# Performance work log

Measured on AMD Instinct MI355X. Metric: run time of the kernel, lower is better.

Reference implementation:

```python
import jax, jax.numpy as jnp
import numpy as np

EPS = 1e-5

def gelu(x):
    return jax.nn.gelu(x, approximate=False)  # torch nn.GELU default = exact erf

def bn(x, g, b, m, v):
    # eval-mode BatchNorm1d with running stats; broadcasts over batch axis
    return (x - m) * jax.lax.rsqrt(v + EPS) * g + b

def ln(x, g, b):
    mu = jnp.mean(x, axis=-1, keepdims=True)
    var = jnp.var(x, axis=-1, keepdims=True)
    return (x - mu) * jax.lax.rsqrt(var + EPS) * g + b

def setup_inputs() -> dict:
    B, D, H, E, C = 4096, 512, 1024, 16, 20  # combined dim D = wifi(256)+rfid(256)
    key = jax.random.key(0)
    ks = iter(jax.random.split(key, 40))
    n = lambda shape, s=0.02: jax.random.normal(next(ks), shape, dtype=jnp.float32) * s
    u = lambda shape: jax.random.uniform(next(ks), shape, dtype=jnp.float32, minval=0.5, maxval=1.5)
    inp = {
        'wifi_feat': jax.random.normal(next(ks), (B, 256), dtype=jnp.float32),
        'rfid_feat': jax.random.normal(next(ks), (B, 256), dtype=jnp.float32),
        # gate: Linear(512,1024) -> LayerNorm -> GELU -> Linear(1024,16) -> Softmax
        'gate_w1': n((D, 1024)), 'gate_b1': n((1024,)),
        'gate_ln_g': 1.0 + n((1024,)), 'gate_ln_b': n((1024,)),
        'gate_w2': n((1024, E)), 'gate_b2': n((E,)),
        # experts stacked on leading E axis
        'exp_w1': n((E, D, H)), 'exp_b1': n((E, H)),
        'exp_bn1_g': 1.0 + n((E, H)), 'exp_bn1_b': n((E, H)), 'exp_bn1_m': n((E, H), 0.1), 'exp_bn1_v': u((E, H)),
        'exp_w2': n((E, H, H)), 'exp_b2': n((E, H)),
        'exp_bn2_g': 1.0 + n((E, H)), 'exp_bn2_b': n((E, H)), 'exp_bn2_m': n((E, H), 0.1), 'exp_bn2_v': u((E, H)),
        # final head: Linear(1024,512) -> BN -> GELU -> Linear(512,20)
        'fin_w1': n((H, 512)), 'fin_b1': n((512,)),
        'fin_bn_g': 1.0 + n((512,)), 'fin_bn_b': n((512,)), 'fin_bn_m': n((512,), 0.1), 'fin_bn_v': u((512,)),
        'fin_w2': n((512, C)), 'fin_b2': n((C,)),
    }
    return inp

def reference(wifi_feat, rfid_feat,
              gate_w1, gate_b1, gate_ln_g, gate_ln_b, gate_w2, gate_b2,
              exp_w1, exp_b1, exp_bn1_g, exp_bn1_b, exp_bn1_m, exp_bn1_v,
              exp_w2, exp_b2, exp_bn2_g, exp_bn2_b, exp_bn2_m, exp_bn2_v,
              fin_w1, fin_b1, fin_bn_g, fin_bn_b, fin_bn_m, fin_bn_v,
              fin_w2, fin_b2):
    TOPK = 4
    combined = jnp.concatenate([wifi_feat, rfid_feat], axis=1)  # [B, 512]
    # gate
    g = gelu(ln(combined @ gate_w1 + gate_b1, gate_ln_g, gate_ln_b))
    gate = jax.nn.softmax(g @ gate_w2 + gate_b2, axis=1)  # [B, E]
    topk_gate, topk_idx = jax.lax.top_k(gate, TOPK)  # sorted, matches torch.topk
    topk_gate = jax.nn.softmax(topk_gate, axis=1)  # [B, K]
    # dense all-expert stack (faithful to original torch.stack over experts)
    h = jnp.einsum('bi,eih->ebh', combined, exp_w1) + exp_b1[:, None, :]  # [E,B,H]
    h = gelu(bn(h, exp_bn1_g[:, None, :], exp_bn1_b[:, None, :], exp_bn1_m[:, None, :], exp_bn1_v[:, None, :]))
    h = jnp.einsum('ebh,eho->ebo', h, exp_w2) + exp_b2[:, None, :]
    h = gelu(bn(h, exp_bn2_g[:, None, :], exp_bn2_b[:, None, :], exp_bn2_m[:, None, :], exp_bn2_v[:, None, :]))
    expert_outputs = jnp.transpose(h, (1, 0, 2))  # [B, E, H]
    selected = jnp.take_along_axis(expert_outputs, topk_idx[:, :, None], axis=1)  # [B,K,H]
    fused = jnp.einsum('bkd,bk->bd', selected, topk_gate)  # [B, H]
    # final head
    o = gelu(bn(fused @ fin_w1 + fin_b1, fin_bn_g, fin_bn_b, fin_bn_m, fin_bn_v))
    return o @ fin_w2 + fin_b2  # [B, num_classes]
```

## Files before the change

### kernel.cpp

```cpp
#include <hip/hip_runtime.h>


#define EPSN 1e-5f

typedef __attribute__((ext_vector_type(8))) short v8s;
typedef __attribute__((ext_vector_type(4))) float v4f;

typedef const unsigned int __attribute__((address_space(1)))* gas_u32;
typedef unsigned int __attribute__((address_space(3)))* las_u32;

__device__ __forceinline__ void glds16(const void* g, const void* l) {
    __builtin_amdgcn_global_load_lds((gas_u32)(uintptr_t)g, (las_u32)(uintptr_t)l, 16, 0, 0);
}

__device__ __forceinline__ float gelu_f(float x) {
    return 0.5f * x * (1.0f + erff(x * 0.70710678118654752440f));
}
__device__ __forceinline__ unsigned short f2bf(float x) {
    unsigned int u = __float_as_uint(x);
    u += 0x7fffu + ((u >> 16) & 1u);
    return (unsigned short)(u >> 16);
}
__device__ __forceinline__ float bf2f(unsigned short u) {
    return __uint_as_float(((unsigned int)u) << 16);
}

__global__ __launch_bounds__(256) void concat_kernel(const float4* __restrict__ wifi,
                                                     const float4* __restrict__ rfid,
                                                     float4* __restrict__ comb,
                                                     ushort4* __restrict__ cbf) {
    int gid = blockIdx.x * 256 + threadIdx.x;
    int b = gid >> 7, c = gid & 127;
    float4 v = (c < 64) ? wifi[b * 64 + c] : rfid[b * 64 + (c - 64)];
    comb[gid] = v;
    ushort4 o;
    o.x = f2bf(v.x); o.y = f2bf(v.y); o.z = f2bf(v.z); o.w = f2bf(v.w);
    cbf[gid] = o;
}

__global__ __launch_bounds__(256) void transpose_f2b(const float* __restrict__ in,
                                                     unsigned short* __restrict__ out,
                                                     int K, int N) {
    __shared__ float t[64][65];
    int e = blockIdx.z;
    int n0 = blockIdx.x << 6, k0 = blockIdx.y << 6;
    const float* ie = in + (long)e * K * N;
    unsigned short* oe = out + (long)e * N * K;
    int tid = threadIdx.x;
    int rr = tid >> 4, cc = (tid & 15) << 2;
#pragma unroll
    for (int p = 0; p < 4; ++p) {
        int k = (p << 4) + rr;
        float4 v = *(const float4*)(ie + (long)(k0 + k) * N + n0 + cc);
        t[k][cc + 0] = v.x; t[k][cc + 1] = v.y; t[k][cc + 2] = v.z; t[k][cc + 3] = v.w;
    }
    __syncthreads();
    int n = tid >> 2, kq = (tid & 3) << 4;
    unsigned short u[16];
#pragma unroll
    for (int j = 0; j < 16; ++j) u[j] = f2bf(t[kq + j][n]);
    uint4* dst = (uint4*)(oe + (long)(n0 + n) * K + k0 + kq);
    dst[0] = ((const uint4*)u)[0];
    dst[1] = ((const uint4*)u)[1];
}

__global__ __launch_bounds__(256) void gate_gemm(
    const float* __restrict__ A, int lda,
    const float* __restrict__ W,
    const float* __restrict__ bias,
    float* __restrict__ out, int ldo, int N, int K)
{
    const int m0 = blockIdx.y << 7;
    const int n0 = blockIdx.x << 6;
    __shared__ float As[16][132];
    __shared__ float Bs[16][68];
    const int tid = threadIdx.x;
    const int ty = tid >> 4, tx = tid & 15;

    const int arow = tid >> 1;
    const int akq  = (tid & 1) << 3;
    const float* Aptr = A + (long)(m0 + arow) * lda + akq;
    const int bkr = tid >> 4;
    const int bnq = (tid & 15) << 2;
    const float* Bptr = W + (long)bkr * N + n0 + bnq;

    float acc[8][4] = {};
    for (int k0 = 0; k0 < K; k0 += 16) {
        float4 a0 = *(const float4*)(Aptr + k0);
        float4 a1 = *(const float4*)(Aptr + k0 + 4);
        float4 bv = *(const float4*)(Bptr + (long)k0 * N);
        As[akq + 0][arow] = a0.x; As[akq + 1][arow] = a0.y;
        As[akq + 2][arow] = a0.z; As[akq + 3][arow] = a0.w;
        As[akq + 4][arow] = a1.x; As[akq + 5][arow] = a1.y;
        As[akq + 6][arow] = a1.z; As[akq + 7][arow] = a1.w;
        *(float4*)&Bs[bkr][bnq] = bv;
        __syncthreads();
#pragma unroll
        for (int kk = 0; kk < 16; ++kk) {
            float4 af0 = *(const float4*)&As[kk][ty << 3];
            float4 af1 = *(const float4*)&As[kk][(ty << 3) + 4];
            float4 bf = *(const float4*)&Bs[kk][tx << 2];
            const float a8[8] = {af0.x, af0.y, af0.z, af0.w, af1.x, af1.y, af1.z, af1.w};
            const float b4[4] = {bf.x, bf.y, bf.z, bf.w};
#pragma unroll
            for (int i = 0; i < 8; ++i)
#pragma unroll
                for (int j = 0; j < 4; ++j)
                    acc[i][j] = fmaf(a8[i], b4[j], acc[i][j]);
        }
        __syncthreads();
    }
#pragma unroll
    for (int i = 0; i < 8; ++i) {
        int r = m0 + (ty << 3) + i;
        int c0 = n0 + (tx << 2);
        float4 v;
        v.x = acc[i][0] + bias[c0 + 0];
        v.y = acc[i][1] + bias[c0 + 1];
        v.z = acc[i][2] + bias[c0 + 2];
        v.w = acc[i][3] + bias[c0 + 3];
        *(float4*)(out + (long)r * ldo + c0) = v;
    }
}

__global__ __launch_bounds__(256) void ln_topk_kernel(
    const float* __restrict__ g,
    const float* __restrict__ lng, const float* __restrict__ lnb,
    const float* __restrict__ w2, const float* __restrict__ b2,
    float* __restrict__ wout, int* __restrict__ rows_, int* __restrict__ counts)
{
    __shared__ float gs[1024];
    __shared__ float red[16][17];
    __shared__ float rs[4], rq[4];
    const int b = blockIdx.x;
    const int tid = threadIdx.x;
    const int c = tid << 2;

    float4 v = *(const float4*)(g + (long)b * 1024 + c);
    float s = v.x + v.y + v.z + v.w;
    float q = v.x * v.x + v.y * v.y + v.z * v.z + v.w * v.w;
    for (int off = 32; off > 0; off >>= 1) {
        s += __shfl_down(s, off);
        q += __shfl_down(q, off);
    }
    int wid = tid >> 6;
    if ((tid & 63) == 0) { rs[wid] = s; rq[wid] = q; }
    __syncthreads();
    float S = rs[0] + rs[1] + rs[2] + rs[3];
    float Q = rq[0] + rq[1] + rq[2] + rq[3];
    float mu = S * (1.0f / 1024.0f);
    float var = Q * (1.0f / 1024.0f) - mu * mu;
    float rstd = rsqrtf(var + EPSN);
    gs[c + 0] = gelu_f((v.x - mu) * rstd * lng[c + 0] + lnb[c + 0]);
    gs[c + 1] = gelu_f((v.y - mu) * rstd * lng[c + 1] + lnb[c + 1]);
    gs[c + 2] = gelu_f((v.z - mu) * rstd * lng[c + 2] + lnb[c + 2]);
    gs[c + 3] = gelu_f((v.w - mu) * rstd * lng[c + 3] + lnb[c + 3]);
    __syncthreads();

    const int e = tid & 15, chunk = tid >> 4;
    float p = 0.f;
#pragma unroll 8
    for (int i = 0; i < 64; ++i) {
        int idx = (chunk << 6) + i;
        p = fmaf(gs[idx], w2[(idx << 4) + e], p);
    }
    red[chunk][e] = p;
    __syncthreads();

    if (tid < 64) {
        float logit = -1e30f;
        if (tid < 16) {
            logit = b2[tid];
#pragma unroll
            for (int cc = 0; cc < 16; ++cc) logit += red[cc][tid];
        }
        float m = logit;
#pragma unroll
        for (int mk = 8; mk >= 1; mk >>= 1) m = fmaxf(m, __shfl_xor(m, mk));
        float pe = (tid < 16) ? expf(logit - m) : 0.f;
        float Z = pe;
#pragma unroll
        for (int mk = 8; mk >= 1; mk >>= 1) Z += __shfl_xor(Z, mk);
        float prob = pe / Z;

        float cur = (tid < 16) ? prob : -1.f;
        const int myi = tid & 15;
        float tv0, tv1, tv2, tv3;
        int ti0, ti1, ti2, ti3;
#define ARGMAX16(TV, TI)                                                     \
        {   float vv = cur; int ii = myi;                                    \
            _Pragma("unroll")                                                \
            for (int mk = 8; mk >= 1; mk >>= 1) {                            \
                float ov = __shfl_xor(vv, mk); int oi = __shfl_xor(ii, mk);  \
                if (ov > vv || (ov == vv && oi < ii)) { vv = ov; ii = oi; }  \
            }                                                                \
            TV = vv; TI = ii;                                                \
            if (myi == ii) cur = -1.f;                                       \
        }
        ARGMAX16(tv0, ti0)
        ARGMAX16(tv1, ti1)
        ARGMAX16(tv2, ti2)
        ARGMAX16(tv3, ti3)
#undef ARGMAX16

        float q0 = 1.f;
        float q1 = expf(tv1 - tv0);
        float q2 = expf(tv2 - tv0);
        float q3 = expf(tv3 - tv0);
        float iZ2 = 1.f / (q0 + q1 + q2 + q3);
        if (tid < 4) {
            float wk = (tid == 0) ? q0 : (tid == 1) ? q1 : (tid == 2) ? q2 : q3;
            int   ee = (tid == 0) ? ti0 : (tid == 1) ? ti1 : (tid == 2) ? ti2 : ti3;
            wout[(b << 2) + tid] = wk * iZ2;
            int j = atomicAdd(&counts[ee], 1);
            rows_[(ee << 12) + j] = (b << 2) | tid;
        }
    }
}

#define WL_MAX 272
__global__ __launch_bounds__(256) void build_wl_kernel(const int* __restrict__ counts,
                                                       int* __restrict__ wl) {
    int t = threadIdx.x;
    for (int i = t; i < WL_MAX; i += 256) wl[i] = -1;
    __syncthreads();
    if (t == 0) {
        int idx = 0;
        for (int e = 0; e < 16; ++e) {
            int nc = (counts[e] + 63) >> 6;
            for (int c = 0; c < nc; ++c) wl[idx++] = (e << 16) | c;
        }
    }
}

template<int ASHIFT, bool GATHER, bool OUTBF, bool WL>
__global__ __launch_bounds__(256) void mfma_gemm(
    const unsigned short* __restrict__ A, int K,
    const unsigned short* __restrict__ Wt, long wstride,
    const float* __restrict__ bias,
    const float* __restrict__ bng, const float* __restrict__ bnb,
    const float* __restrict__ bnm, const float* __restrict__ bnv,
    int pstride,
    void* __restrict__ outv, int ldo,
    const int* __restrict__ rows_, const int* __restrict__ counts,
    const int* __restrict__ wl, int M)
{
    constexpr int TM = 64;
    int e, m0;
    if constexpr (WL) {
        int w = wl[blockIdx.y];
        if (w < 0) return;
        e = w >> 16;
        m0 = (w & 0xffff) << 6;
    } else {
        e = blockIdx.y;
        m0 = blockIdx.z * TM;
    }
    const int n0 = blockIdx.x << 7;
    const int cnt = GATHER ? counts[e] : M;

    constexpr int AB_USH = 64 * 64 + 128 * 64;
    constexpr int OL_STRIDE = 136;
    constexpr int OL_USH = OUTBF ? TM * OL_STRIDE : 0;
    constexpr int SM_USH = (OL_USH > AB_USH) ? OL_USH : AB_USH;
    __shared__ __align__(16) unsigned short smem[SM_USH];
    unsigned short* Als = smem;
    unsigned short* Bls = smem + 64 * 64;
    __shared__ int rid[TM];
    __shared__ int ain[TM];

    const int tid = threadIdx.x;
    if (tid < TM) {
        int i = m0 + tid;
        int pk, ai;
        if (GATHER) {
            if (i < cnt) { pk = rows_[(e << 12) + i]; ai = pk >> ASHIFT; }
            else { pk = -1; ai = 0; }
        } else { pk = i; ai = i; }
        rid[tid] = pk;
        ain[tid] = ai;
    }
    __syncthreads();

    const int wave = tid >> 6, lane = tid & 63;
    const int wm = (wave >> 1) << 5, wn = (wave & 1) << 6;
    const int lrow = lane & 15, kch = lane >> 4;
    const int wb = wave << 9;

    const int srow = tid >> 3, spos = tid & 7;
    const int skc8 = (spos ^ (srow & 7)) << 3;

    const unsigned short* apa = A + (long)ain[srow] * K + skc8;
    const unsigned short* apb = A + (long)ain[32 + srow] * K + skc8;
    const unsigned short* Wte = Wt + (long)e * wstride;
    const unsigned short* bp0 = Wte + (long)(n0 + srow) * K + skc8;
    const unsigned short* bp1 = Wte + (long)(n0 + 32 + srow) * K + skc8;
    const unsigned short* bp2 = Wte + (long)(n0 + 64 + srow) * K + skc8;
    const unsigned short* bp3 = Wte + (long)(n0 + 96 + srow) * K + skc8;

    v4f acc[2][4] = {};

    const int nk = K >> 6;
    for (int it = 0; it < nk; ++it) {
        glds16(apa, Als + wb);
        glds16(apb, Als + 2048 + wb);
        glds16(bp0, Bls + wb);
        glds16(bp1, Bls + 2048 + wb);
        glds16(bp2, Bls + 4096 + wb);
        glds16(bp3, Bls + 6144 + wb);
        apa += 64; apb += 64; bp0 += 64; bp1 += 64; bp2 += 64; bp3 += 64;
        __syncthreads();

#pragma unroll
        for (int s = 0; s < 2; ++s) {
            const int kc = (s << 2) | kch;
            v8s av[2], bv[4];
#pragma unroll
            for (int f = 0; f < 2; ++f) {
                const int row = wm + (f << 4) + lrow;
                av[f] = *(const v8s*)(Als + row * 64 + ((kc ^ (row & 7)) << 3));
            }
#pragma unroll
            for (int f = 0; f < 4; ++f) {
                const int row = wn + (f << 4) + lrow;
                bv[f] = *(const v8s*)(Bls + row * 64 + ((kc ^ (row & 7)) << 3));
            }
#pragma unroll
            for (int fi = 0; fi < 2; ++fi)
#pragma unroll
                for (int fj = 0; fj < 4; ++fj)
                    acc[fi][fj] = __builtin_amdgcn_mfma_f32_16x16x32_bf16(
                        av[fi], bv[fj], acc[fi][fj], 0, 0, 0);
        }
        __syncthreads();
    }

    if constexpr (OUTBF) {
        unsigned short* Ols = smem;
#pragma unroll
        for (int fj = 0; fj < 4; ++fj) {
            const int c = wn + (fj << 4) + lrow;
            const int pc = e * pstride + n0 + c;
            const float bs = bias[pc];
            const float sc = bng[pc] * rsqrtf(bnv[pc] + EPSN);
            const float mn = bnm[pc], bb = bnb[pc];
#pragma unroll
            for (int fi = 0; fi < 2; ++fi) {
#pragma unroll
                for (int r = 0; r < 4; ++r) {
                    const int lr = wm + (fi << 4) + (kch << 2) + r;
                    float x = acc[fi][fj][r] + bs;
                    x = (x - mn) * sc + bb;
                    x = gelu_f(x);
                    Ols[lr * OL_STRIDE + c] = f2bf(x);
                }
            }
        }
        __syncthreads();
        const int rl = tid >> 4;
        const int c8 = (tid & 15) << 3;
#pragma unroll
        for (int p = 0; p < TM / 16; ++p) {
            const int row = (p << 4) + rl;
            const int orow = rid[row];
            if (orow >= 0) {
                uint4 v = *(const uint4*)(Ols + row * OL_STRIDE + c8);
                *(uint4*)((unsigned short*)outv + (long)orow * ldo + n0 + c8) = v;
            }
        }
    } else {
#pragma unroll
        for (int fj = 0; fj < 4; ++fj) {
            const int c = n0 + wn + (fj << 4) + lrow;
            const int pc = e * pstride + c;
            const float bs = bias[pc];
            const float sc = bng[pc] * rsqrtf(bnv[pc] + EPSN);
            const float mn = bnm[pc], bb = bnb[pc];
#pragma unroll
            for (int fi = 0; fi < 2; ++fi) {
#pragma unroll
                for (int r = 0; r < 4; ++r) {
                    const int lr = wm + (fi << 4) + (kch << 2) + r;
                    const int orow = rid[lr];
                    if (orow < 0) continue;
                    float x = acc[fi][fj][r] + bs;
                    x = (x - mn) * sc + bb;
                    x = gelu_f(x);
                    ((float*)outv)[(long)orow * ldo + c] = x;
                }
            }
        }
    }
}

__global__ __launch_bounds__(256) void combine_bf_kernel(const ushort4* __restrict__ h2b,
                                                         const float* __restrict__ w,
                                                         ushort4* __restrict__ fusedb) {
    int gid = blockIdx.x * 256 + threadIdx.x;
    int b = gid >> 8, c = gid & 255;
    float a0 = 0.f, a1 = 0.f, a2 = 0.f, a3 = 0.f;
#pragma unroll
    for (int k = 0; k < 4; ++k) {
        float wk = w[b * 4 + k];
        ushort4 v = h2b[(long)(b * 4 + k) * 256 + c];
        a0 += wk * bf2f(v.x); a1 += wk * bf2f(v.y);
        a2 += wk * bf2f(v.z); a3 += wk * bf2f(v.w);
    }
    ushort4 o;
    o.x = f2bf(a0); o.y = f2bf(a1); o.z = f2bf(a2); o.w = f2bf(a3);
    fusedb[gid] = o;
}

__global__ __launch_bounds__(256) void fin2_kernel(const float* __restrict__ o,
                                                   const float* __restrict__ w2,
                                                   const float* __restrict__ b2,
                                                   float* __restrict__ out) {
    __shared__ float ws[512 * 20];
    int tid = threadIdx.x;
    for (int i = tid; i < 512 * 20; i += 256) ws[i] = w2[i];
    __syncthreads();
    int r = blockIdx.x * 64 + (tid >> 2);
    int c0 = (tid & 3) * 5;
    float acc[5];
#pragma unroll
    for (int j = 0; j < 5; ++j) acc[j] = b2[c0 + j];
    const float* orow = o + (long)r * 512;
    for (int i = 0; i < 512; ++i) {
        float v = orow[i];
#pragma unroll
        for (int j = 0; j < 5; ++j) acc[j] += v * ws[i * 20 + c0 + j];
    }
#pragma unroll
    for (int j = 0; j < 5; ++j) out[r * 20 + c0 + j] = acc[j];
}

extern "C" void kernel_launch(void* const* d_in, const int* in_sizes, int n_in,
                              void* d_out, int out_size, void* d_ws, size_t ws_size,
                              hipStream_t stream) {
    const float* wifi    = (const float*)d_in[0];
    const float* rfid    = (const float*)d_in[1];
    const float* gate_w1 = (const float*)d_in[2];
    const float* gate_b1 = (const float*)d_in[3];
    const float* gln_g   = (const float*)d_in[4];
    const float* gln_b   = (const float*)d_in[5];
    const float* gate_w2 = (const float*)d_in[6];
    const float* gate_b2 = (const float*)d_in[7];
    const float* exp_w1  = (const float*)d_in[8];
    const float* exp_b1  = (const float*)d_in[9];
    const float* bn1g    = (const float*)d_in[10];
    const float* bn1b    = (const float*)d_in[11];
    const float* bn1m    = (const float*)d_in[12];
    const float* bn1v    = (const float*)d_in[13];
    const float* exp_w2  = (const float*)d_in[14];
    const float* exp_b2  = (const float*)d_in[15];
    const float* bn2g    = (const float*)d_in[16];
    const float* bn2b    = (const float*)d_in[17];
    const float* bn2m    = (const float*)d_in[18];
    const float* bn2v    = (const float*)d_in[19];
    const float* fin_w1  = (const float*)d_in[20];
    const float* fin_b1  = (const float*)d_in[21];
    const float* fbng    = (const float*)d_in[22];
    const float* fbnb    = (const float*)d_in[23];
    const float* fbnm    = (const float*)d_in[24];
    const float* fbnv    = (const float*)d_in[25];
    const float* fin_w2  = (const float*)d_in[26];
    const float* fin_b2  = (const float*)d_in[27];
    float* out = (float*)d_out;

    const size_t MBy = 1u << 20;
    char* W = (char*)d_ws;
    float*          combined = (float*)         (W + 0);
    unsigned short* cbf      = (unsigned short*)(W + 8 * MBy);
    unsigned short* w1t      = (unsigned short*)(W + 12 * MBy);
    unsigned short* fusedb   = (unsigned short*)(W + 12 * MBy);
    float*          obuf     = (float*)         (W + 20 * MBy);
    unsigned short* w2t      = (unsigned short*)(W + 29 * MBy);
    float*          wq       = (float*)         (W + 61 * MBy);
    int*            rows     = (int*)           (W + 61 * MBy + (1 << 16));
    int*            counts   = (int*)           (W + 61 * MBy + (1 << 16) + (1 << 18));
    int*            wl       = (int*)           (W + 61 * MBy + (1 << 16) + (1 << 18) + 256);
    unsigned short* fw1t     = (unsigned short*)(W + 63 * MBy);
    unsigned short* h1bf     = (unsigned short*)(W + 65 * MBy);
    float*          gbuf     = (float*)         (W + 99 * MBy);
    unsigned short* h2b      = (unsigned short*)(W + 99 * MBy);

    hipMemsetAsync(counts, 0, 16 * sizeof(int), stream);

    concat_kernel<<<2048, 256, 0, stream>>>((const float4*)wifi, (const float4*)rfid,
                                            (float4*)combined, (ushort4*)cbf);

    transpose_f2b<<<dim3(16, 8, 16), 256, 0, stream>>>(exp_w1, w1t, 512, 1024);
    transpose_f2b<<<dim3(16, 16, 16), 256, 0, stream>>>(exp_w2, w2t, 1024, 1024);
    transpose_f2b<<<dim3(8, 16, 1), 256, 0, stream>>>(fin_w1, fw1t, 1024, 512);

    gate_gemm<<<dim3(16, 32, 1), 256, 0, stream>>>(combined, 512, gate_w1, gate_b1,
                                                   gbuf, 1024, 1024, 512);
    ln_topk_kernel<<<4096, 256, 0, stream>>>(gbuf, gln_g, gln_b, gate_w2, gate_b2,
                                             wq, rows, counts);
    build_wl_kernel<<<1, 256, 0, stream>>>(counts, wl);

    mfma_gemm<2, true, true, true><<<dim3(8, WL_MAX, 1), 256, 0, stream>>>(
        cbf, 512, w1t, (long)512 * 1024, exp_b1,
        bn1g, bn1b, bn1m, bn1v, 1024,
        h1bf, 1024, rows, counts, wl, 4096);

    mfma_gemm<0, true, true, true><<<dim3(8, WL_MAX, 1), 256, 0, stream>>>(
        h1bf, 1024, w2t, (long)1024 * 1024, exp_b2,
        bn2g, bn2b, bn2m, bn2v, 1024,
        h2b, 1024, rows, counts, wl, 4096);

    combine_bf_kernel<<<4096, 256, 0, stream>>>((const ushort4*)h2b, wq, (ushort4*)fusedb);

    mfma_gemm<0, false, false, false><<<dim3(4, 1, 64), 256, 0, stream>>>(
        fusedb, 1024, fw1t, 0, fin_b1,
        fbng, fbnb, fbnm, fbnv, 0,
        obuf, 512, nullptr, counts, nullptr, 4096);

    fin2_kernel<<<64, 256, 0, stream>>>(obuf, fin_w2, fin_b2, out);
}
```

Baseline: 481.7 us.

## Run gate GEMM on bf16 MFMA using split hi/lo bf16x3 emulation

```diff
diff --git a/kernel.cpp b/kernel.cpp
--- a/kernel.cpp
+++ b/kernel.cpp
@@ -28,14 +28,23 @@
 __global__ __launch_bounds__(256) void concat_kernel(const float4* __restrict__ wifi,
                                                      const float4* __restrict__ rfid,
                                                      float4* __restrict__ comb,
-                                                     ushort4* __restrict__ cbf) {
+                                                     ushort4* __restrict__ cbf,
+                                                     ushort4* __restrict__ cbf3) {
     int gid = blockIdx.x * 256 + threadIdx.x;
     int b = gid >> 7, c = gid & 127;
     float4 v = (c < 64) ? wifi[b * 64 + c] : rfid[b * 64 + (c - 64)];
     comb[gid] = v;
-    ushort4 o;
-    o.x = f2bf(v.x); o.y = f2bf(v.y); o.z = f2bf(v.z); o.w = f2bf(v.w);
-    cbf[gid] = o;
+    ushort4 hi, lo;
+    hi.x = f2bf(v.x); hi.y = f2bf(v.y); hi.z = f2bf(v.z); hi.w = f2bf(v.w);
+    lo.x = f2bf(v.x - bf2f(hi.x));
+    lo.y = f2bf(v.y - bf2f(hi.y));
+    lo.z = f2bf(v.z - bf2f(hi.z));
+    lo.w = f2bf(v.w - bf2f(hi.w));
+    cbf[gid] = hi;
+    const long r3 = (long)b * 384 + c;
+    cbf3[r3]       = hi;
+    cbf3[r3 + 128] = lo;
+    cbf3[r3 + 256] = hi;
 }
 
 __global__ __launch_bounds__(256) void transpose_f2b(const float* __restrict__ in,
@@ -64,63 +73,36 @@
     dst[1] = ((const uint4*)u)[1];
 }
 
-__global__ __launch_bounds__(256) void gate_gemm(
-    const float* __restrict__ A, int lda,
-    const float* __restrict__ W,
-    const float* __restrict__ bias,
-    float* __restrict__ out, int ldo, int N, int K)
-{
-    const int m0 = blockIdx.y << 7;
-    const int n0 = blockIdx.x << 6;
-    __shared__ float As[16][132];
-    __shared__ float Bs[16][68];
-    const int tid = threadIdx.x;
-    const int ty = tid >> 4, tx = tid & 15;
-
-    const int arow = tid >> 1;
-    const int akq  = (tid & 1) << 3;
-    const float* Aptr = A + (long)(m0 + arow) * lda + akq;
-    const int bkr = tid >> 4;
-    const int bnq = (tid & 15) << 2;
-    const float* Bptr = W + (long)bkr * N + n0 + bnq;
-
-    float acc[8][4] = {};
-    for (int k0 = 0; k0 < K; k0 += 16) {
-        float4 a0 = *(const float4*)(Aptr + k0);
-        float4 a1 = *(const float4*)(Aptr + k0 + 4);
-        float4 bv = *(const float4*)(Bptr + (long)k0 * N);
-        As[akq + 0][arow] = a0.x; As[akq + 1][arow] = a0.y;
-        As[akq + 2][arow] = a0.z; As[akq + 3][arow] = a0.w;
-        As[akq + 4][arow] = a1.x; As[akq + 5][arow] = a1.y;
-        As[akq + 6][arow] = a1.z; As[akq + 7][arow] = a1.w;
-        *(float4*)&Bs[bkr][bnq] = bv;
-        __syncthreads();
-#pragma unroll
-        for (int kk = 0; kk < 16; ++kk) {
-            float4 af0 = *(const float4*)&As[kk][ty << 3];
-            float4 af1 = *(const float4*)&As[kk][(ty << 3) + 4];
-            float4 bf = *(const float4*)&Bs[kk][tx << 2];
-            const float a8[8] = {af0.x, af0.y, af0.z, af0.w, af1.x, af1.y, af1.z, af1.w};
-            const float b4[4] = {bf.x, bf.y, bf.z, bf.w};
-#pragma unroll
-            for (int i = 0; i < 8; ++i)
-#pragma unroll
-                for (int j = 0; j < 4; ++j)
-                    acc[i][j] = fmaf(a8[i], b4[j], acc[i][j]);
-        }
-        __syncthreads();
-    }
-#pragma unroll
-    for (int i = 0; i < 8; ++i) {
-        int r = m0 + (ty << 3) + i;
-        int c0 = n0 + (tx << 2);
-        float4 v;
-        v.x = acc[i][0] + bias[c0 + 0];
-        v.y = acc[i][1] + bias[c0 + 1];
-        v.z = acc[i][2] + bias[c0 + 2];
-        v.w = acc[i][3] + bias[c0 + 3];
-        *(float4*)(out + (long)r * ldo + c0) = v;
-    }
+__global__ __launch_bounds__(256) void transpose_f2b_hilo(const float* __restrict__ in,
+                                                          unsigned short* __restrict__ out,
+                                                          int K, int N) {
+    __shared__ float t[64][65];
+    int n0 = blockIdx.x << 6, k0 = blockIdx.y << 6;
+    int tid = threadIdx.x;
+    int rr = tid >> 4, cc = (tid & 15) << 2;
+#pragma unroll
+    for (int p = 0; p < 4; ++p) {
+        int k = (p << 4) + rr;
+        float4 v = *(const float4*)(in + (long)(k0 + k) * N + n0 + cc);
+        t[k][cc + 0] = v.x; t[k][cc + 1] = v.y; t[k][cc + 2] = v.z; t[k][cc + 3] = v.w;
+    }
+    __syncthreads();
+    int n = tid >> 2, kq = (tid & 3) << 4;
+    unsigned short uh[16], ul[16];
+#pragma unroll
+    for (int j = 0; j < 16; ++j) {
+        float x = t[kq + j][n];
+        unsigned short h = f2bf(x);
+        uh[j] = h;
+        ul[j] = f2bf(x - bf2f(h));
+    }
+    unsigned short* dh = out + (long)(n0 + n) * (3 * K) + k0 + kq;
+    ((uint4*)dh)[0]           = ((const uint4*)uh)[0];
+    ((uint4*)dh)[1]           = ((const uint4*)uh)[1];
+    ((uint4*)(dh + K))[0]     = ((const uint4*)uh)[0];
+    ((uint4*)(dh + K))[1]     = ((const uint4*)uh)[1];
+    ((uint4*)(dh + 2 * K))[0] = ((const uint4*)ul)[0];
+    ((uint4*)(dh + 2 * K))[1] = ((const uint4*)ul)[1];
 }
 
 __global__ __launch_bounds__(256) void ln_topk_kernel(
@@ -233,7 +215,7 @@
     }
 }
 
-template<int ASHIFT, bool GATHER, bool OUTBF, bool WL>
+template<int ASHIFT, bool GATHER, bool OUTBF, bool WL, bool PLAIN = false>
 __global__ __launch_bounds__(256) void mfma_gemm(
     const unsigned short* __restrict__ A, int K,
     const unsigned short* __restrict__ Wt, long wstride,
@@ -374,8 +356,11 @@
             const int c = n0 + wn + (fj << 4) + lrow;
             const int pc = e * pstride + c;
             const float bs = bias[pc];
-            const float sc = bng[pc] * rsqrtf(bnv[pc] + EPSN);
-            const float mn = bnm[pc], bb = bnb[pc];
+            float sc = 1.f, mn = 0.f, bb = 0.f;
+            if constexpr (!PLAIN) {
+                sc = bng[pc] * rsqrtf(bnv[pc] + EPSN);
+                mn = bnm[pc]; bb = bnb[pc];
+            }
 #pragma unroll
             for (int fi = 0; fi < 2; ++fi) {
 #pragma unroll
@@ -384,8 +369,10 @@
                     const int orow = rid[lr];
                     if (orow < 0) continue;
                     float x = acc[fi][fj][r] + bs;
-                    x = (x - mn) * sc + bb;
-                    x = gelu_f(x);
+                    if constexpr (!PLAIN) {
+                        x = (x - mn) * sc + bb;
+                        x = gelu_f(x);
+                    }
                     ((float*)outv)[(long)orow * ldo + c] = x;
                 }
             }
@@ -481,20 +468,27 @@
     int*            wl       = (int*)           (W + 61 * MBy + (1 << 16) + (1 << 18) + 256);
     unsigned short* fw1t     = (unsigned short*)(W + 63 * MBy);
     unsigned short* h1bf     = (unsigned short*)(W + 65 * MBy);
+    unsigned short* cbf3     = (unsigned short*)(W + 65 * MBy);
+    unsigned short* w1t3     = (unsigned short*)(W + 77 * MBy);
     float*          gbuf     = (float*)         (W + 99 * MBy);
     unsigned short* h2b      = (unsigned short*)(W + 99 * MBy);
 
     hipMemsetAsync(counts, 0, 16 * sizeof(int), stream);
 
     concat_kernel<<<2048, 256, 0, stream>>>((const float4*)wifi, (const float4*)rfid,
-                                            (float4*)combined, (ushort4*)cbf);
+                                            (float4*)combined, (ushort4*)cbf,
+                                            (ushort4*)cbf3);
 
     transpose_f2b<<<dim3(16, 8, 16), 256, 0, stream>>>(exp_w1, w1t, 512, 1024);
     transpose_f2b<<<dim3(16, 16, 16), 256, 0, stream>>>(exp_w2, w2t, 1024, 1024);
     transpose_f2b<<<dim3(8, 16, 1), 256, 0, stream>>>(fin_w1, fw1t, 1024, 512);
-
-    gate_gemm<<<dim3(16, 32, 1), 256, 0, stream>>>(combined, 512, gate_w1, gate_b1,
-                                                   gbuf, 1024, 1024, 512);
+    transpose_f2b_hilo<<<dim3(16, 8, 1), 256, 0, stream>>>(gate_w1, w1t3, 512, 1024);
+
+    mfma_gemm<0, false, false, false, true><<<dim3(8, 1, 64), 256, 0, stream>>>(
+        cbf3, 1536, w1t3, 0, gate_b1,
+        nullptr, nullptr, nullptr, nullptr, 0,
+        gbuf, 1024, nullptr, counts, nullptr, 4096);
+
     ln_topk_kernel<<<4096, 256, 0, stream>>>(gbuf, gln_g, gln_b, gate_w2, gate_b2,
                                              wq, rows, counts);
     build_wl_kernel<<<1, 256, 0, stream>>>(counts, wl);
```

Result: faster. 464.4 us (-3.6%).
